# Kernel tuning notes

Hardware: AMD Instinct MI355X
Metric: run time of the kernel (lower is better)

Reference implementation:

```python
import jax, jax.numpy as jnp
import numpy as np

B, S, C, HEADS, EXP = 8, 1024, 256, 8, 4
H = W = 32  # S = H*W
HID = EXP * C
RATES = (1, 6, 12, 18)
EPS = 1e-5


def _conv(x, w, b=None, dilation=1, padding=0):
    out = jax.lax.conv_general_dilated(
        x, w, (1, 1), [(padding, padding), (padding, padding)],
        rhs_dilation=(dilation, dilation),
        dimension_numbers=('NCHW', 'OIHW', 'NCHW'))
    if b is not None:
        out = out + b[None, :, None, None]
    return out


def _bn(x, g, b, m, v):
    # inference-mode BatchNorm2d
    s = (g / jnp.sqrt(v + EPS))[None, :, None, None]
    return (x - m[None, :, None, None]) * s + b[None, :, None, None]


def _ln(x, g, b):
    mu = jnp.mean(x, -1, keepdims=True)
    var = jnp.mean((x - mu) ** 2, -1, keepdims=True)
    return (x - mu) / jnp.sqrt(var + EPS) * g + b


def setup_inputs() -> dict:
    key = jax.random.key(0)
    ks = iter(jax.random.split(key, 64))

    def n(shape, s=0.05):
        return jax.random.normal(next(ks), shape, jnp.float32) * s

    def u(shape):
        return jax.random.uniform(next(ks), shape, jnp.float32, 0.5, 1.5)

    inp = {
        'value': n((B, S, C), 1.0),
        'key': n((B, S, C), 1.0),
        'query': n((B, S, C), 1.0),
        'res': n((B, S, C), 1.0),
        # nn.MultiheadAttention params
        'attn_wi': n((3 * C, C)), 'attn_bi': jnp.zeros((3 * C,)),
        'attn_wo': n((C, C)), 'attn_bo': jnp.zeros((C,)),
        # Modulator params
        'mod_bias': jnp.zeros((1, C, 1, 1)),
        'ca_w1': n((C // 16, C)), 'ca_w2': n((C, C // 16)),
        'pa_w': n((C, C, 1, 1)),
        'pa_bn_g': jnp.ones((C,)), 'pa_bn_b': jnp.zeros((C,)),
        'pa_bn_m': n((C,), 0.1), 'pa_bn_v': u((C,)),
        'sa_w': n((4, C, C, 3, 3)), 'sa_b': jnp.zeros((4, C)),
        'sa_bn_g': jnp.ones((4, C)), 'sa_bn_b': jnp.zeros((4, C)),
        'sa_bn_m': n((4, C), 0.1), 'sa_bn_v': u((4, C)),
        'sa_out_w': n((C, 4 * C, 1, 1)), 'sa_out_b': jnp.zeros((C,)),
        'out_w': n((C, C, 1, 1)), 'out_b': jnp.zeros((C,)),
        'out_bn_g': jnp.ones((C,)), 'out_bn_b': jnp.zeros((C,)),
        'out_bn_m': n((C,), 0.1), 'out_bn_v': u((C,)),
        # LayerNorms
        'ln1_g': jnp.ones((C,)), 'ln1_b': jnp.zeros((C,)),
        'ln2_g': jnp.ones((C,)), 'ln2_b': jnp.zeros((C,)),
        # E_MLP params
        'mlp_w1': n((HID, C)), 'mlp_b1': jnp.zeros((HID,)),
        'dw_w': n((HID, HID, 3, 3), 0.02), 'dw_b': jnp.zeros((HID,)),
        'pw_w': n((HID, HID, 3, 3), 0.02), 'pw_b': jnp.zeros((HID,)),
        'mlp_w2': n((C, HID)), 'mlp_b2': jnp.zeros((C,)),
    }
    return inp


def reference(value, key, query, res,
              attn_wi, attn_bi, attn_wo, attn_bo,
              mod_bias, ca_w1, ca_w2, pa_w,
              pa_bn_g, pa_bn_b, pa_bn_m, pa_bn_v,
              sa_w, sa_b, sa_bn_g, sa_bn_b, sa_bn_m, sa_bn_v,
              sa_out_w, sa_out_b, out_w, out_b,
              out_bn_g, out_bn_b, out_bn_m, out_bn_v,
              ln1_g, ln1_b, ln2_g, ln2_b,
              mlp_w1, mlp_b1, dw_w, dw_b, pw_w, pw_b, mlp_w2, mlp_b2):
    d = C // HEADS
    # SMA arg shuffle: block calls sma(query,key,value) -> SMA(value=query,key=key,query=value)
    # -> nn.MultiheadAttention(query=value_blk, key=key_blk, value=query_blk)
    q = (value @ attn_wi[:C].T + attn_bi[:C]).reshape(B, S, HEADS, d)
    k = (key @ attn_wi[C:2 * C].T + attn_bi[C:2 * C]).reshape(B, S, HEADS, d)
    v = (query @ attn_wi[2 * C:].T + attn_bi[2 * C:]).reshape(B, S, HEADS, d)
    scores = jnp.einsum('bqhd,bkhd->bhqk', q, k) / jnp.sqrt(jnp.float32(d))
    attn = jax.nn.softmax(scores, axis=-1)
    ctx = jnp.einsum('bhqk,bkhd->bqhd', attn, v).reshape(B, S, C)
    msa = ctx @ attn_wo.T + attn_bo                       # [B,S,C]

    x = msa.transpose(0, 2, 1).reshape(B, C, H, W)        # [B,C,H,W]

    # --- Modulator ---
    pa = x * jax.nn.sigmoid(_bn(_conv(x, pa_w), pa_bn_g, pa_bn_b, pa_bn_m, pa_bn_v))
    y = jnp.mean(x, axis=(2, 3))                          # [B,C]
    y = jax.nn.sigmoid(jax.nn.relu(y @ ca_w1.T) @ ca_w2.T)
    ca = x * y[:, :, None, None]
    pa_ca = jax.nn.softmax(pa @ ca, axis=-1)              # [B,C,H,H] (H==W)
    sa_outs = [_bn(jax.nn.relu(_conv(x, sa_w[i], sa_b[i], dilation=r, padding=r)),
                   sa_bn_g[i], sa_bn_b[i], sa_bn_m[i], sa_bn_v[i])
               for i, r in enumerate(RATES)]
    sa = _conv(jnp.concatenate(sa_outs, axis=1), sa_out_w, sa_out_b)
    out = pa_ca @ sa                                      # [B,C,H,W]
    out = _bn(_conv(out, out_w, out_b), out_bn_g, out_bn_b, out_bn_m, out_bn_v)
    syn = out + mod_bias + x                              # residual inside modulator

    attn_seq = syn.reshape(B, C, S).transpose(0, 2, 1)    # [B,S,C]
    q2 = _ln(attn_seq + res, ln1_g, ln1_b)

    # --- E_MLP ---
    h = jax.nn.gelu(q2 @ mlp_w1.T + mlp_b1, approximate=False)  # [B,S,4C]
    hc = h.transpose(0, 2, 1).reshape(B, HID, H, W)
    hc = _conv(hc, dw_w, dw_b, padding=1)
    hc = _conv(hc, pw_w, pw_b, padding=1)
    h2 = hc.reshape(B, HID, S).transpose(0, 2, 1)
    ff = h2 @ mlp_w2.T + mlp_b2
    return _ln(ff + q2, ln2_g, ln2_b)
```

## Files before the change

kernel.cpp:

```cpp
#include <hip/hip_runtime.h>
#include <hip/hip_bf16.h>
#include <math.h>

typedef __attribute__((ext_vector_type(8))) short bf16x8;
typedef __attribute__((ext_vector_type(4))) short bf16x4;
typedef __attribute__((ext_vector_type(4))) float f32x4;

#define MM 8192
#define CC 256

__device__ __forceinline__ short f2bf(float f) {
  unsigned u = __float_as_uint(f);
  u = (u + 0x7FFFu + ((u >> 16) & 1u)) >> 16;
  return (short)u;
}

__device__ __forceinline__ void gload16(const short* g, short* l) {
  __builtin_amdgcn_global_load_lds(
      (const __attribute__((address_space(1))) unsigned int*)(g),
      (__attribute__((address_space(3))) unsigned int*)(l), 16, 0, 0);
}

__global__ __launch_bounds__(256, 2) void convh_k(const short* __restrict__ Ain,
                                                  const short* __restrict__ Wt,
                                                  short* __restrict__ outB,
                                                  const float* __restrict__ bias) {
  extern __shared__ short sm[];
  const int tid = threadIdx.x;
  const int bx = blockIdx.x;
  const int bm = bx & 63, bn = bx >> 6;
  const int l = tid & 63, w = tid >> 6;
  const int wm = w >> 1, wn = w & 1;
  const int lr = l & 15, lg = l >> 4;
  const int lsub = l >> 3;
  const int srcu = (l & 7) ^ lsub;
  const int img = bm >> 3, rbase = (bm & 7) * 4;
  const bf16x8 zv = {0, 0, 0, 0, 0, 0, 0, 0};

  f32x4 acc[4][4];
#pragma unroll
  for (int i = 0; i < 4; ++i)
#pragma unroll
    for (int j = 0; j < 4; ++j) acc[i][j] = (f32x4){0.f, 0.f, 0.f, 0.f};

  const short* wsrc[4];
#pragma unroll
  for (int i = 0; i < 4; ++i) {
    int rowi = (w * 4 + i) * 8 + lsub;
    wsrc[i] = Wt + (size_t)(bn * 128 + rowi) * 1024 + srcu * 8;
  }

  const short* asrc[6]; int apos[6]; bool avalid[6];
#pragma unroll
  for (int i = 0; i < 6; ++i) {
    int ug = tid + i * 256;
    int pos = ug >> 3, u = ug & 7;
    int irow = pos >> 5, px = pos & 31;
    int grow = rbase + irow - 1;
    avalid[i] = ((unsigned)grow < 32u);
    int growc = grow < 0 ? 0 : (grow > 31 ? 31 : grow);
    asrc[i] = Ain + ((size_t)(img * 1024 + growc * 32 + px)) * 1024 + u * 8;
    apos[i] = pos * 64 + ((u ^ (pos & 7)) << 3);
  }

  bf16x8 areg[6];
  auto issueA = [&](int kc) {
#pragma unroll
    for (int i = 0; i < 6; ++i)
      areg[i] = *(const bf16x8*)(asrc[i] + kc * 64);
  };
  auto writeA = [&](int ab) {
    short* abuf = sm + 16384 + ab * 12288;
#pragma unroll
    for (int i = 0; i < 6; ++i)
      *(bf16x8*)(abuf + apos[i]) = avalid[i] ? areg[i] : zv;
  };
  auto issueW = [&](int kc, int tap, int wb) {
    short* base = sm + wb * 8192;
    size_t wo = (size_t)tap * 1048576 + (size_t)kc * 64;
#pragma unroll
    for (int i = 0; i < 4; ++i)
      gload16(wsrc[i] + wo, base + (w * 4 + i) * 512);
  };
  auto compute = [&](int dy, int dx, const short* bA, const short* bB) {
    __builtin_amdgcn_s_setprio(1);
#pragma unroll
    for (int ks = 0; ks < 64; ks += 32) {
      const int u = (ks >> 3) + lg;
      bf16x8 af[4], bfr[4];
#pragma unroll
      for (int mt = 0; mt < 4; ++mt) {
        int px = (mt & 1) * 16 + lr;
        int ipx = px + dx;
        bool okx = ((unsigned)ipx < 32u);
        int pos = (wm * 2 + (mt >> 1) + 1 + dy) * 32 + (ipx & 31);
        bf16x8 v = *(const bf16x8*)&bA[pos * 64 + ((u ^ (pos & 7)) << 3)];
        af[mt] = okx ? v : zv;
      }
#pragma unroll
      for (int nt = 0; nt < 4; ++nt)
        bfr[nt] = *(const bf16x8*)&bB[(wn * 64 + nt * 16 + lr) * 64 + ((u ^ (lr & 7)) << 3)];
#pragma unroll
      for (int mt = 0; mt < 4; ++mt)
#pragma unroll
        for (int nt = 0; nt < 4; ++nt)
          acc[mt][nt] = __builtin_amdgcn_mfma_f32_16x16x32_bf16(af[mt], bfr[nt], acc[mt][nt], 0, 0, 0);
    }
    __builtin_amdgcn_s_setprio(0);
  };

  issueA(0);
  issueW(0, 0, 0);
  issueW(0, 1, 1);
  asm volatile("s_waitcnt vmcnt(4)" ::: "memory");
  writeA(0);
  asm volatile("s_waitcnt lgkmcnt(0)" ::: "memory");

  for (int kc = 0; kc < 16; ++kc) {
    const int ab = kc & 1;
    const short* bA = sm + 16384 + ab * 12288;
#pragma unroll
    for (int tap = 0; tap < 9; ++tap) {
      const int wb = (kc + tap) & 1;
      const short* bB = sm + wb * 8192;
      if (tap == 7) {
        if (kc < 15) asm volatile("s_waitcnt vmcnt(10)" ::: "memory");
        else         asm volatile("s_waitcnt vmcnt(4)" ::: "memory");
      } else if (tap == 8) {
        if (kc < 15) asm volatile("s_waitcnt vmcnt(4)" ::: "memory");
        else         asm volatile("s_waitcnt vmcnt(0)" ::: "memory");
      } else {
        asm volatile("s_waitcnt vmcnt(4)" ::: "memory");
      }
      asm volatile("s_barrier" ::: "memory");
      compute(tap / 3 - 1, tap % 3 - 1, bA, bB);
      asm volatile("s_barrier" ::: "memory");
      if (tap <= 6) {
        if (tap == 6 && kc < 15) issueA(kc + 1);
        issueW(kc, tap + 2, wb);
      } else if (tap == 7) {
        if (kc < 15) issueW(kc + 1, 0, wb);
      } else {
        if (kc < 15) {
          writeA(ab ^ 1);
          asm volatile("s_waitcnt lgkmcnt(0)" ::: "memory");
          issueW(kc + 1, 1, wb);
        }
      }
    }
  }

#pragma unroll
  for (int nt = 0; nt < 4; ++nt) {
    const int col = bn * 128 + wn * 64 + nt * 16 + lr;
    const float bi = bias[col];
#pragma unroll
    for (int mt = 0; mt < 4; ++mt) {
      const int row0 = bm * 128 + wm * 64 + mt * 16 + lg * 4;
#pragma unroll
      for (int j = 0; j < 4; ++j)
        outB[(size_t)(row0 + j) * 1024 + col] = f2bf(acc[mt][nt][j] + bi);
    }
  }
}

struct GP {
  const short* A; const short* W; float* outF; short* outB;
  const float* bias; const float* scale; const float* shift; const float* aux;
  const short* zero;
  long aZStride, wZStride, oZStride;
  int N, Kc, ldA, ldOut, outColOff, outZOff;
  int dil0, dil1, dil2, dil3;
  int T, nkcs;
};

template<int TAPS, int EPI, int OUTMODE>
__global__ __launch_bounds__(256, 2) void gemmd_k(GP p) {
  extern __shared__ short sm[];
  const int tid = threadIdx.x;
  const int bx = blockIdx.x, bz = blockIdx.z;
  const int bm = bx & 63, bn = bx >> 6;
  const int l = tid & 63, w = tid >> 6;
  const int wm = w >> 1, wn = w & 1;
  const int lr = l & 15, lg = l >> 4;
  const int lsub = l >> 3;
  const int srcu = (l & 7) ^ lsub;

  const short* Abase = p.A + (size_t)bz * p.aZStride;
  const short* Wbase = p.W + (size_t)bz * p.wZStride;
  const int dil = (TAPS == 9)
      ? (bz == 0 ? p.dil0 : bz == 1 ? p.dil1 : bz == 2 ? p.dil2 : p.dil3) : 1;

  f32x4 acc[4][4];
#pragma unroll
  for (int i = 0; i < 4; ++i)
#pragma unroll
    for (int j = 0; j < 4; ++j) acc[i][j] = (f32x4){0.f, 0.f, 0.f, 0.f};

  int rowi[4], prow[4], bimg[4], py[4], px[4];
  const short* wsrc[4];
#pragma unroll
  for (int i = 0; i < 4; ++i) {
    rowi[i] = (w * 4 + i) * 8 + lsub;
    prow[i] = bm * 128 + rowi[i];
    bimg[i] = prow[i] >> 10; py[i] = (prow[i] >> 5) & 31; px[i] = prow[i] & 31;
    wsrc[i] = Wbase + (size_t)(bn * 128 + rowi[i]) * p.Kc + srcu * 8;
  }
  const size_t wTap = (size_t)p.N * p.Kc;
  const int nkcMask = (1 << p.nkcs) - 1;

  auto issue = [&](int t, int buf) {
    const int tap = t >> p.nkcs;
    const int kc = t & nkcMask;
    short* base = sm + buf * 16384;
    if (TAPS == 1) {
#pragma unroll
      for (int i = 0; i < 4; ++i)
        gload16(Abase + (size_t)prow[i] * p.ldA + kc * 64 + srcu * 8,
                base + (w * 4 + i) * 512);
    } else {
      const int dy = (tap / 3 - 1) * dil, dx = (tap % 3 - 1) * dil;
#pragma unroll
      for (int i = 0; i < 4; ++i) {
        int yy = py[i] + dy, xx = px[i] + dx;
        bool ok = ((unsigned)yy < 32u) & ((unsigned)xx < 32u);
        const short* a = ok
            ? Abase + (size_t)((bimg[i] << 10) + (yy << 5) + xx) * p.ldA + kc * 64
            : p.zero;
        gload16(a + srcu * 8, base + (w * 4 + i) * 512);
      }
    }
    short* bbase = base + 8192;
    const size_t wo = (size_t)tap * wTap + kc * 64;
#pragma unroll
    for (int i = 0; i < 4; ++i)
      gload16(wsrc[i] + wo, bbase + (w * 4 + i) * 512);
  };

  auto compute = [&](int buf) {
    const short* bA = sm + buf * 16384;
    const short* bB = bA + 8192;
    __builtin_amdgcn_s_setprio(1);
#pragma unroll
    for (int ks = 0; ks < 64; ks += 32) {
      const int u = (ks >> 3) + lg;
      bf16x8 af[4], bfr[4];
#pragma unroll
      for (int mt = 0; mt < 4; ++mt)
        af[mt] = *(bf16x8*)&bA[(wm * 64 + mt * 16 + lr) * 64 + ((u ^ (lr & 7)) << 3)];
#pragma unroll
      for (int nt = 0; nt < 4; ++nt)
        bfr[nt] = *(bf16x8*)&bB[(wn * 64 + nt * 16 + lr) * 64 + ((u ^ (lr & 7)) << 3)];
#pragma unroll
      for (int mt = 0; mt < 4; ++mt)
#pragma unroll
        for (int nt = 0; nt < 4; ++nt)
          acc[mt][nt] = __builtin_amdgcn_mfma_f32_16x16x32_bf16(af[mt], bfr[nt], acc[mt][nt], 0, 0, 0);
    }
    __builtin_amdgcn_s_setprio(0);
  };

  issue(0, 0);
  if (p.T > 1) issue(1, 1);
  int cur = 0;
  for (int t = 0; t < p.T; ++t) {
    if (t + 1 < p.T) asm volatile("s_waitcnt vmcnt(8)" ::: "memory");
    else             asm volatile("s_waitcnt vmcnt(0)" ::: "memory");
    asm volatile("s_barrier" ::: "memory");
    compute(cur);
    asm volatile("s_barrier" ::: "memory");
    if (t + 2 < p.T) issue(t + 2, cur);
    cur ^= 1;
  }

  float* outF = p.outF + (size_t)bz * p.oZStride;
  short* outB = p.outB + (size_t)bz * p.oZStride;
#pragma unroll
  for (int nt = 0; nt < 4; ++nt) {
    const int col = bn * 128 + wn * 64 + nt * 16 + lr;
    const int gcol = p.outColOff + bz * p.outZOff + col;
    const float bi = (p.bias != nullptr) ? p.bias[bz * p.N + col] : 0.f;
    float scl = 0.f, shf = 0.f;
    if (EPI == 3 || EPI == 4 || EPI == 5) {
      scl = p.scale[bz * p.N + col]; shf = p.shift[bz * p.N + col];
    }
#pragma unroll
    for (int mt = 0; mt < 4; ++mt) {
      const int row0 = bm * 128 + wm * 64 + mt * 16 + lg * 4;
#pragma unroll
      for (int j = 0; j < 4; ++j) {
        const long row = row0 + j;
        float v = acc[mt][nt][j];
        if (EPI == 1 || EPI == 2 || EPI == 3) v += bi;
        if (EPI == 2) v = 0.5f * v * (1.f + erff(v * 0.70710678118654752f));
        if (EPI == 3) { v = fmaxf(v, 0.f); v = v * scl + shf; }
        if (EPI == 4) {
          float t2 = v * scl + shf;
          float sg = 1.f / (1.f + __expf(-t2));
          v = p.aux[row * 256 + col] * sg;
        }
        if (EPI == 5) v = v * scl + shf + p.aux[row * 256 + col];
        if (OUTMODE == 0 || OUTMODE == 2) outF[row * (long)p.ldOut + gcol] = v;
        if (OUTMODE == 1 || OUTMODE == 2) outB[row * (long)p.ldOut + gcol] = f2bf(v);
      }
    }
  }
}

__global__ __launch_bounds__(256) void attn_k(const short* qb, const short* kb,
                                              const short* vb, short* ctx) {
  __shared__ short lK[128 * 40];
  __shared__ short lVt[32 * 136];
  __shared__ short lP[4][16 * 136];
  const int tid = threadIdx.x;
  const int qt = blockIdx.x;
  const int bh = blockIdx.y;
  const int b = bh >> 3, h = bh & 7;
  const int l = tid & 63, wv = tid >> 6;
  const int lr = l & 15, lg = l >> 4;
  const float SC = 0.17677669529663687f;

  const int qrow = qt * 64 + wv * 16 + lr;
  const bf16x8 qf = *(const bf16x8*)(qb + ((size_t)(b * 1024 + qrow)) * 256 + h * 32 + lg * 8);

  f32x4 o0 = {0.f,0.f,0.f,0.f}, o1 = {0.f,0.f,0.f,0.f};
  float m[4] = {-1e30f, -1e30f, -1e30f, -1e30f};
  float lsum[4] = {0.f, 0.f, 0.f, 0.f};

  for (int ch = 0; ch < 8; ++ch) {
    __syncthreads();
    {
      const int keyi = tid >> 1, d0 = (tid & 1) * 16;
      const short* src = kb + ((size_t)(b * 1024 + ch * 128 + keyi)) * 256 + h * 32 + d0;
      short* dst = &lK[keyi * 40 + d0];
      *(bf16x8*)dst = *(const bf16x8*)src;
      *(bf16x8*)(dst + 8) = *(const bf16x8*)(src + 8);
    }
    {
      const int keyi = tid >> 1, d0 = (tid & 1) * 16;
      const short* src = vb + ((size_t)(b * 1024 + ch * 128 + keyi)) * 256 + h * 32 + d0;
      short tmp[16];
      *(bf16x8*)tmp = *(const bf16x8*)src;
      *(bf16x8*)(tmp + 8) = *(const bf16x8*)(src + 8);
#pragma unroll
      for (int j = 0; j < 16; ++j) lVt[(d0 + j) * 136 + keyi] = tmp[j];
    }
    __syncthreads();

    f32x4 sc[8];
#pragma unroll
    for (int jt = 0; jt < 8; ++jt) {
      bf16x8 bfr = *(bf16x8*)&lK[(jt * 16 + lr) * 40 + lg * 8];
      sc[jt] = __builtin_amdgcn_mfma_f32_16x16x32_bf16(qf, bfr, (f32x4){0.f,0.f,0.f,0.f}, 0, 0, 0);
      sc[jt] *= SC;
    }
#pragma unroll
    for (int j = 0; j < 4; ++j) {
      float rm = -1e30f;
#pragma unroll
      for (int jt = 0; jt < 8; ++jt) rm = fmaxf(rm, sc[jt][j]);
      rm = fmaxf(rm, __shfl_xor(rm, 1));
      rm = fmaxf(rm, __shfl_xor(rm, 2));
      rm = fmaxf(rm, __shfl_xor(rm, 4));
      rm = fmaxf(rm, __shfl_xor(rm, 8));
      float mn = fmaxf(m[j], rm);
      float alpha = exp2f((m[j] - mn) * 1.44269504088896f);
      m[j] = mn;
      float rs = 0.f;
#pragma unroll
      for (int jt = 0; jt < 8; ++jt) {
        float pv = exp2f((sc[jt][j] - mn) * 1.44269504088896f);
        sc[jt][j] = pv;
        rs += pv;
      }
      rs += __shfl_xor(rs, 1); rs += __shfl_xor(rs, 2);
      rs += __shfl_xor(rs, 4); rs += __shfl_xor(rs, 8);
      lsum[j] = lsum[j] * alpha + rs;
      o0[j] *= alpha; o1[j] *= alpha;
      const int prw = lg * 4 + j;
#pragma unroll
      for (int jt = 0; jt < 8; ++jt) lP[wv][prw * 136 + jt * 16 + lr] = f2bf(sc[jt][j]);
    }
#pragma unroll
    for (int kc = 0; kc < 4; ++kc) {
      bf16x8 pf = *(bf16x8*)&lP[wv][lr * 136 + kc * 32 + lg * 8];
      bf16x8 v0 = *(bf16x8*)&lVt[lr * 136 + kc * 32 + lg * 8];
      bf16x8 v1 = *(bf16x8*)&lVt[(16 + lr) * 136 + kc * 32 + lg * 8];
      o0 = __builtin_amdgcn_mfma_f32_16x16x32_bf16(pf, v0, o0, 0, 0, 0);
      o1 = __builtin_amdgcn_mfma_f32_16x16x32_bf16(pf, v1, o1, 0, 0, 0);
    }
  }
  const size_t orow = (size_t)(b * 1024 + qt * 64 + wv * 16);
#pragma unroll
  for (int j = 0; j < 4; ++j) {
    float inv = 1.f / lsum[j];
    ctx[(orow + lg * 4 + j) * 256 + h * 32 + lr]      = f2bf(o0[j] * inv);
    ctx[(orow + lg * 4 + j) * 256 + h * 32 + 16 + lr] = f2bf(o1[j] * inv);
  }
}

__global__ __launch_bounds__(256) void cvt4_k(const float* src, short* dst, int n4) {
  int i = blockIdx.x * 256 + threadIdx.x;
  if (i < n4) {
    f32x4 v = ((const f32x4*)src)[i];
    bf16x4 o;
    o[0] = f2bf(v[0]); o[1] = f2bf(v[1]); o[2] = f2bf(v[2]); o[3] = f2bf(v[3]);
    ((bf16x4*)dst)[i] = o;
  }
}

__global__ __launch_bounds__(256) void zero_k(short* p) {
  p[blockIdx.x * 256 + threadIdx.x] = 0;
}

__global__ __launch_bounds__(256) void tap_k(const float* src, short* dst, int n) {
  int i = blockIdx.x * 256 + threadIdx.x;
  if (i >= n) return;
  const float* s = src + (size_t)i * 9;
  float v[9];
#pragma unroll
  for (int t = 0; t < 9; ++t) v[t] = s[t];
#pragma unroll
  for (int t = 0; t < 9; ++t) dst[(size_t)t * n + i] = f2bf(v[t]);
}

__global__ void bnprep_k(const float* pg, const float* pb, const float* pm, const float* pv,
                         const float* sg, const float* sb, const float* sm, const float* sv,
                         const float* og, const float* ob, const float* om, const float* ov,
                         const float* conv_ob, const float* mbias, float* out) {
  int c = threadIdx.x;
  float s = pg[c] / sqrtf(pv[c] + 1e-5f);
  out[c] = s;
  out[256 + c] = pb[c] - pm[c] * s;
  for (int i = 0; i < 4; ++i) {
    int idx = i * 256 + c;
    float ss = sg[idx] / sqrtf(sv[idx] + 1e-5f);
    out[512 + idx] = ss;
    out[1536 + idx] = sb[idx] - sm[idx] * ss;
  }
  float os = og[c] / sqrtf(ov[c] + 1e-5f);
  out[2560 + c] = os;
  out[2816 + c] = ob[c] - om[c] * os + conv_ob[c] * os + mbias[c];
}

__global__ __launch_bounds__(256) void tposef_k(const float* src, float* dst) {
  __shared__ float tile[32][33];
  int pc = blockIdx.x, cc = blockIdx.y, b = blockIdx.z;
  int tx = threadIdx.x & 31, ty = threadIdx.x >> 5;
  const float* s = src + ((size_t)b * 1024 + pc * 32) * 256 + cc * 32;
#pragma unroll
  for (int k = 0; k < 4; ++k)
    tile[ty + 8 * k][tx] = s[(ty + 8 * k) * 256 + tx];
  __syncthreads();
  float* d = dst + ((size_t)b * 256 + cc * 32) * 1024 + pc * 32;
#pragma unroll
  for (int k = 0; k < 4; ++k)
    d[(ty + 8 * k) * 1024 + tx] = tile[tx][ty + 8 * k];
}

__global__ __launch_bounds__(256) void tposeb_k(const float* src, short* dst) {
  __shared__ float tile[32][33];
  int pc = blockIdx.x, cc = blockIdx.y, b = blockIdx.z;
  int tx = threadIdx.x & 31, ty = threadIdx.x >> 5;
  const float* s = src + ((size_t)b * 256 + cc * 32) * 1024 + pc * 32;
#pragma unroll
  for (int k = 0; k < 4; ++k)
    tile[ty + 8 * k][tx] = s[(ty + 8 * k) * 1024 + tx];
  __syncthreads();
  short* d = dst + ((size_t)b * 1024 + pc * 32) * 256 + cc * 32;
#pragma unroll
  for (int k = 0; k < 4; ++k)
    d[(ty + 8 * k) * 256 + tx] = f2bf(tile[tx][ty + 8 * k]);
}

__global__ __launch_bounds__(256) void camean_k(const float* x, float* partial) {
  int blk = blockIdx.x, c = threadIdx.x;
  const float* px = x + ((size_t)blk * 64) * 256 + c;
  float s = 0.f;
#pragma unroll 4
  for (int r = 0; r < 64; ++r) s += px[(size_t)r * 256];
  partial[blk * 256 + c] = s;
}

__global__ __launch_bounds__(256) void ca2_k(const float* partial, const float* w1,
                                             const float* w2, float* y2) {
  __shared__ float ly[256];
  __shared__ float ly1[16];
  int b = blockIdx.x, c = threadIdx.x;
  float s = 0.f;
#pragma unroll
  for (int j = 0; j < 16; ++j) s += partial[(b * 16 + j) * 256 + c];
  ly[c] = s * (1.f / 1024.f);
  __syncthreads();
  if (c < 16) {
    float a = 0.f;
    const float* wp = w1 + c * 256;
    for (int i = 0; i < 256; ++i) a += ly[i] * wp[i];
    ly1[c] = fmaxf(a, 0.f);
  }
  __syncthreads();
  float a = 0.f;
  const float* wp = w2 + c * 16;
#pragma unroll
  for (int j = 0; j < 16; ++j) a += ly1[j] * wp[j];
  y2[b * 256 + c] = 1.f / (1.f + __expf(-a));
}

__global__ __launch_bounds__(256) void bm1_k(const float* paT, const float* xT,
                                             const float* y2, float* pa_ca) {
  __shared__ float sp[32][33], sx[32][33], so[32][33];
  __shared__ float rinv[32];
  int bc = blockIdx.x, t = threadIdx.x;
  for (int e = t; e < 1024; e += 256) {
    sp[e >> 5][e & 31] = paT[(size_t)bc * 1024 + e];
    sx[e >> 5][e & 31] = xT[(size_t)bc * 1024 + e];
  }
  __syncthreads();
  float yv = y2[bc];
  int i = t >> 3, j0 = (t & 7) * 4;
  float a0 = 0.f, a1 = 0.f, a2 = 0.f, a3 = 0.f;
  for (int k = 0; k < 32; ++k) {
    float pv = sp[i][k];
    a0 += pv * sx[k][j0];     a1 += pv * sx[k][j0 + 1];
    a2 += pv * sx[k][j0 + 2]; a3 += pv * sx[k][j0 + 3];
  }
  so[i][j0] = a0 * yv; so[i][j0 + 1] = a1 * yv;
  so[i][j0 + 2] = a2 * yv; so[i][j0 + 3] = a3 * yv;
  __syncthreads();
  if (t < 32) {
    float mx = -1e30f;
    for (int j = 0; j < 32; ++j) mx = fmaxf(mx, so[t][j]);
    float sum = 0.f;
    for (int j = 0; j < 32; ++j) { float pp = __expf(so[t][j] - mx); so[t][j] = pp; sum += pp; }
    rinv[t] = 1.f / sum;
  }
  __syncthreads();
  for (int e = t; e < 1024; e += 256)
    pa_ca[(size_t)bc * 1024 + e] = so[e >> 5][e & 31] * rinv[e >> 5];
}

__global__ __launch_bounds__(256) void bm2_k(const float* pa_ca, const float* saT, float* moT) {
  __shared__ float sp[32][33], ss[32][33];
  int bc = blockIdx.x, t = threadIdx.x;
  for (int e = t; e < 1024; e += 256) {
    sp[e >> 5][e & 31] = pa_ca[(size_t)bc * 1024 + e];
    ss[e >> 5][e & 31] = saT[(size_t)bc * 1024 + e];
  }
  __syncthreads();
  int i = t >> 3, j0 = (t & 7) * 4;
  float a0 = 0.f, a1 = 0.f, a2 = 0.f, a3 = 0.f;
  for (int k = 0; k < 32; ++k) {
    float pv = sp[i][k];
    a0 += pv * ss[k][j0];     a1 += pv * ss[k][j0 + 1];
    a2 += pv * ss[k][j0 + 2]; a3 += pv * ss[k][j0 + 3];
  }
  size_t base = (size_t)bc * 1024 + i * 32 + j0;
  moT[base] = a0; moT[base + 1] = a1; moT[base + 2] = a2; moT[base + 3] = a3;
}

template<int DUAL>
__global__ __launch_bounds__(256) void ln_k(const float* in, const float* res,
                                            const float* g, const float* bta,
                                            float* out, short* outB) {
  __shared__ float red[8];
  size_t row = blockIdx.x;
  int c = threadIdx.x;
  int wv = c >> 6, lane = c & 63;
  float v = in[row * 256 + c] + res[row * 256 + c];
  float s = v;
  for (int mk = 1; mk < 64; mk <<= 1) s += __shfl_xor(s, mk);
  if (lane == 0) red[wv] = s;
  __syncthreads();
  float mu = (red[0] + red[1] + red[2] + red[3]) * (1.f / 256.f);
  float d = v - mu;
  float q = d * d;
  for (int mk = 1; mk < 64; mk <<= 1) q += __shfl_xor(q, mk);
  if (lane == 0) red[4 + wv] = q;
  __syncthreads();
  float var = (red[4] + red[5] + red[6] + red[7]) * (1.f / 256.f);
  float o = d * rsqrtf(var + 1e-5f) * g[c] + bta[c];
  out[row * 256 + c] = o;
  if (DUAL) outB[row * 256 + c] = f2bf(o);
}

extern "C" void kernel_launch(void* const* d_in, const int* in_sizes, int n_in,
                              void* d_out, int out_size, void* d_ws, size_t ws_size,
                              hipStream_t stream) {
  (void)in_sizes; (void)n_in; (void)out_size; (void)ws_size;
  const float* value    = (const float*)d_in[0];
  const float* key      = (const float*)d_in[1];
  const float* query    = (const float*)d_in[2];
  const float* res      = (const float*)d_in[3];
  const float* attn_wi  = (const float*)d_in[4];
  const float* attn_bi  = (const float*)d_in[5];
  const float* attn_wo  = (const float*)d_in[6];
  const float* attn_bo  = (const float*)d_in[7];
  const float* mod_bias = (const float*)d_in[8];
  const float* ca_w1    = (const float*)d_in[9];
  const float* ca_w2    = (const float*)d_in[10];
  const float* pa_w     = (const float*)d_in[11];
  const float* pa_bn_g  = (const float*)d_in[12];
  const float* pa_bn_b  = (const float*)d_in[13];
  const float* pa_bn_m  = (const float*)d_in[14];
  const float* pa_bn_v  = (const float*)d_in[15];
  const float* sa_w     = (const float*)d_in[16];
  const float* sa_b     = (const float*)d_in[17];
  const float* sa_bn_g  = (const float*)d_in[18];
  const float* sa_bn_b  = (const float*)d_in[19];
  const float* sa_bn_m  = (const float*)d_in[20];
  const float* sa_bn_v  = (const float*)d_in[21];
  const float* sa_out_w = (const float*)d_in[22];
  const float* sa_out_b = (const float*)d_in[23];
  const float* out_w    = (const float*)d_in[24];
  const float* out_b    = (const float*)d_in[25];
  const float* out_bn_g = (const float*)d_in[26];
  const float* out_bn_b = (const float*)d_in[27];
  const float* out_bn_m = (const float*)d_in[28];
  const float* out_bn_v = (const float*)d_in[29];
  const float* ln1_g    = (const float*)d_in[30];
  const float* ln1_b    = (const float*)d_in[31];
  const float* ln2_g    = (const float*)d_in[32];
  const float* ln2_b    = (const float*)d_in[33];
  const float* mlp_w1   = (const float*)d_in[34];
  const float* mlp_b1   = (const float*)d_in[35];
  const float* dw_w     = (const float*)d_in[36];
  const float* dw_b     = (const float*)d_in[37];
  const float* pw_w     = (const float*)d_in[38];
  const float* pw_b     = (const float*)d_in[39];
  const float* mlp_w2   = (const float*)d_in[40];
  const float* mlp_b2   = (const float*)d_in[41];

  char* ws = (char*)d_ws;
  const size_t MB = 1024 * 1024;
  char* A = ws + 0 * MB;
  char* Bx = ws + 16 * MB;
  char* Cx = ws + 32 * MB;
  float* xbuf  = (float*)(ws + 40 * MB);
  short* xbf   = (short*)(ws + 48 * MB);
  char* Fx = ws + 52 * MB;
  float* q2buf = (float*)(ws + 60 * MB);
  short* q2B   = (short*)(ws + 68 * MB);
  short* wdw   = (short*)(ws + 72 * MB);
  short* wpw   = (short*)(ws + 90 * MB);
  size_t o = 108 * MB;
  short* w_awi  = (short*)(ws + o); o += 768 * 256 * 2;
  short* w_awo  = (short*)(ws + o); o += 256 * 256 * 2;
  short* w_pa   = (short*)(ws + o); o += 256 * 256 * 2;
  short* w_sa   = (short*)(ws + o); o += (size_t)4 * 9 * 256 * 256 * 2;
  short* w_saou = (short*)(ws + o); o += 256 * 1024 * 2;
  short* w_out  = (short*)(ws + o); o += 256 * 256 * 2;
  short* w_mlp1 = (short*)(ws + o); o += 1024 * 256 * 2;
  short* w_mlp2 = (short*)(ws + o); o += 256 * 1024 * 2;
  float* bn     = (float*)(ws + o); o += 3072 * 4;
  float* y2buf  = (float*)(ws + o); o += 8 * 256 * 4;
  float* capart = (float*)(ws + o); o += 128 * 256 * 4;
  short* zbuf   = (short*)(ws + o); o += 2048 * 2;

  short* vkq  = (short*)A;
  short* qkv  = (short*)Bx;
  short* ctxB = (short*)Cx;
  float* xT   = (float*)A;
  float* paT  = (float*)(A + 8 * MB);
  float* paBuf = (float*)Cx;
  float* pa_ca = (float*)Bx;
  float* saBuf = (float*)(Bx + 8 * MB);
  short* saCat = (short*)A;
  float* saT  = (float*)Cx;
  float* moT  = (float*)Fx;
  short* modB = (short*)Cx;
  float* synBuf = (float*)Fx;
  short* hB   = (short*)A;
  short* hc1B = (short*)Bx;
  short* h2B  = (short*)A;
  float* ffBuf = (float*)Cx;

  const int LDSB = 2 * 16384 * 2;
  const int LDSC = 40960 * 2;
  hipFuncSetAttribute((const void*)gemmd_k<1, 1, 1>, hipFuncAttributeMaxDynamicSharedMemorySize, LDSB);
  hipFuncSetAttribute((const void*)gemmd_k<1, 1, 2>, hipFuncAttributeMaxDynamicSharedMemorySize, LDSB);
  hipFuncSetAttribute((const void*)gemmd_k<1, 4, 0>, hipFuncAttributeMaxDynamicSharedMemorySize, LDSB);
  hipFuncSetAttribute((const void*)gemmd_k<9, 3, 1>, hipFuncAttributeMaxDynamicSharedMemorySize, LDSB);
  hipFuncSetAttribute((const void*)gemmd_k<1, 1, 0>, hipFuncAttributeMaxDynamicSharedMemorySize, LDSB);
  hipFuncSetAttribute((const void*)gemmd_k<1, 5, 0>, hipFuncAttributeMaxDynamicSharedMemorySize, LDSB);
  hipFuncSetAttribute((const void*)gemmd_k<1, 2, 1>, hipFuncAttributeMaxDynamicSharedMemorySize, LDSB);
  hipFuncSetAttribute((const void*)convh_k, hipFuncAttributeMaxDynamicSharedMemorySize, LDSC);

  zero_k<<<8, 256, 0, stream>>>(zbuf);
  cvt4_k<<<192, 256, 0, stream>>>(attn_wi, w_awi, 768 * 64);
  cvt4_k<<<64, 256, 0, stream>>>(attn_wo, w_awo, 256 * 64);
  cvt4_k<<<64, 256, 0, stream>>>(pa_w, w_pa, 256 * 64);
  for (int i4 = 0; i4 < 4; ++i4)
    tap_k<<<256, 256, 0, stream>>>(sa_w + (size_t)i4 * 589824,
                                   w_sa + (size_t)i4 * 589824, 65536);
  cvt4_k<<<256, 256, 0, stream>>>(sa_out_w, w_saou, 1024 * 64);
  cvt4_k<<<64, 256, 0, stream>>>(out_w, w_out, 256 * 64);
  cvt4_k<<<256, 256, 0, stream>>>(mlp_w1, w_mlp1, 1024 * 64);
  cvt4_k<<<256, 256, 0, stream>>>(mlp_w2, w_mlp2, 1024 * 64);
  tap_k<<<4096, 256, 0, stream>>>(dw_w, wdw, 1048576);
  tap_k<<<4096, 256, 0, stream>>>(pw_w, wpw, 1048576);
  bnprep_k<<<1, 256, 0, stream>>>(pa_bn_g, pa_bn_b, pa_bn_m, pa_bn_v,
                                  sa_bn_g, sa_bn_b, sa_bn_m, sa_bn_v,
                                  out_bn_g, out_bn_b, out_bn_m, out_bn_v,
                                  out_b, mod_bias, bn);
  cvt4_k<<<2048, 256, 0, stream>>>(value, vkq, MM * 64);
  cvt4_k<<<2048, 256, 0, stream>>>(key,   vkq + (size_t)MM * 256, MM * 64);
  cvt4_k<<<2048, 256, 0, stream>>>(query, vkq + (size_t)2 * MM * 256, MM * 64);

  GP g;
  g.zero = zbuf; g.scale = nullptr; g.shift = nullptr; g.aux = nullptr;
  g.aZStride = 0; g.wZStride = 0; g.oZStride = 0;
  g.outColOff = 0; g.outZOff = 0;
  g.dil0 = 1; g.dil1 = 1; g.dil2 = 1; g.dil3 = 1;
  g.outF = nullptr; g.outB = nullptr;

  g.A = vkq; g.W = w_awi; g.outB = qkv; g.bias = attn_bi;
  g.N = 256; g.Kc = 256; g.ldA = 256; g.ldOut = 256; g.T = 4; g.nkcs = 2;
  g.aZStride = (size_t)MM * 256; g.wZStride = 256 * 256; g.oZStride = (size_t)MM * 256;
  gemmd_k<1, 1, 1><<<dim3(128, 1, 3), 256, LDSB, stream>>>(g);
  g.aZStride = 0; g.wZStride = 0; g.oZStride = 0;

  attn_k<<<dim3(16, 64), 256, 0, stream>>>(qkv, qkv + (size_t)MM * 256,
                                           qkv + (size_t)2 * MM * 256, ctxB);

  g.A = ctxB; g.W = w_awo; g.outF = xbuf; g.outB = xbf; g.bias = attn_bo;
  gemmd_k<1, 1, 2><<<dim3(128), 256, LDSB, stream>>>(g);

  tposef_k<<<dim3(32, 8, 8), 256, 0, stream>>>(xbuf, xT);

  g.A = xbf; g.W = w_pa; g.outF = paBuf; g.outB = nullptr; g.bias = nullptr;
  g.scale = bn; g.shift = bn + 256; g.aux = xbuf;
  gemmd_k<1, 4, 0><<<dim3(128), 256, LDSB, stream>>>(g);
  g.scale = nullptr; g.shift = nullptr; g.aux = nullptr;
  tposef_k<<<dim3(32, 8, 8), 256, 0, stream>>>(paBuf, paT);

  camean_k<<<128, 256, 0, stream>>>(xbuf, capart);
  ca2_k<<<8, 256, 0, stream>>>(capart, ca_w1, ca_w2, y2buf);
  bm1_k<<<2048, 256, 0, stream>>>(paT, xT, y2buf, pa_ca);

  g.A = xbf; g.W = w_sa; g.outB = saCat; g.outF = nullptr;
  g.bias = sa_b; g.scale = bn + 512; g.shift = bn + 1536;
  g.ldOut = 1024; g.outZOff = 256; g.wZStride = (size_t)9 * 256 * 256;
  g.dil0 = 1; g.dil1 = 6; g.dil2 = 12; g.dil3 = 18;
  g.T = 36; g.nkcs = 2;
  gemmd_k<9, 3, 1><<<dim3(128, 1, 4), 256, LDSB, stream>>>(g);
  g.outZOff = 0; g.wZStride = 0; g.scale = nullptr; g.shift = nullptr;
  g.dil0 = 1; g.dil1 = 1; g.dil2 = 1; g.dil3 = 1;

  g.A = saCat; g.W = w_saou; g.outF = saBuf; g.outB = nullptr; g.bias = sa_out_b;
  g.N = 256; g.Kc = 1024; g.ldA = 1024; g.ldOut = 256; g.T = 16; g.nkcs = 4;
  gemmd_k<1, 1, 0><<<dim3(128), 256, LDSB, stream>>>(g);
  tposef_k<<<dim3(32, 8, 8), 256, 0, stream>>>(saBuf, saT);

  bm2_k<<<2048, 256, 0, stream>>>(pa_ca, saT, moT);
  tposeb_k<<<dim3(32, 8, 8), 256, 0, stream>>>(moT, modB);

  g.A = modB; g.W = w_out; g.outF = synBuf; g.bias = nullptr;
  g.scale = bn + 2560; g.shift = bn + 2816; g.aux = xbuf;
  g.N = 256; g.Kc = 256; g.ldA = 256; g.ldOut = 256; g.T = 4; g.nkcs = 2;
  gemmd_k<1, 5, 0><<<dim3(128), 256, LDSB, stream>>>(g);
  g.scale = nullptr; g.shift = nullptr; g.aux = nullptr;

  ln_k<1><<<8192, 256, 0, stream>>>(synBuf, res, ln1_g, ln1_b, q2buf, q2B);

  g.A = q2B; g.W = w_mlp1; g.outB = hB; g.outF = nullptr; g.bias = mlp_b1;
  g.N = 1024; g.Kc = 256; g.ldA = 256; g.ldOut = 1024; g.T = 4; g.nkcs = 2;
  gemmd_k<1, 2, 1><<<dim3(512), 256, LDSB, stream>>>(g);

  convh_k<<<dim3(512), 256, LDSC, stream>>>(hB, wdw, hc1B, dw_b);

  convh_k<<<dim3(512), 256, LDSC, stream>>>(hc1B, wpw, h2B, pw_b);

  g.A = h2B; g.W = w_mlp2; g.outF = ffBuf; g.outB = nullptr; g.bias = mlp_b2;
  g.N = 256; g.Kc = 1024; g.ldA = 1024; g.ldOut = 256; g.T = 16; g.nkcs = 4;
  gemmd_k<1, 1, 0><<<dim3(128), 256, LDSB, stream>>>(g);

  ln_k<0><<<8192, 256, 0, stream>>>(ffBuf, q2buf, ln2_g, ln2_b, (float*)d_out, nullptr);
}
```

Measured before the change: 579.4 us.

## Load conv weights directly into registers, drop LDS weight staging and barriers

In the 3x3 conv kernel, the weight B-fragments are now read from global memory straight into registers, double-buffered across taps, instead of being staged through LDS with async global-to-LDS loads. Only the activation tile stays in static LDS, which cuts LDS use and removes the two barriers per tap, leaving one barrier per K chunk. Each lane now issues its own uncoalesced-ish 16-byte global loads and needs 16 extra vector registers. It also relies on the compiler's waitcnt placement instead of explicit vmcnt tuning, which may expose global load latency and limit occupancy.

```diff
diff --git a/kernel.cpp b/kernel.cpp
--- a/kernel.cpp
+++ b/kernel.cpp
@@ -25,15 +25,13 @@
                                                   const short* __restrict__ Wt,
                                                   short* __restrict__ outB,
                                                   const float* __restrict__ bias) {
-  extern __shared__ short sm[];
+  __shared__ short sA[2][12288];
   const int tid = threadIdx.x;
   const int bx = blockIdx.x;
   const int bm = bx & 63, bn = bx >> 6;
   const int l = tid & 63, w = tid >> 6;
   const int wm = w >> 1, wn = w & 1;
   const int lr = l & 15, lg = l >> 4;
-  const int lsub = l >> 3;
-  const int srcu = (l & 7) ^ lsub;
   const int img = bm >> 3, rbase = (bm & 7) * 4;
   const bf16x8 zv = {0, 0, 0, 0, 0, 0, 0, 0};
 
@@ -43,12 +41,7 @@
 #pragma unroll
     for (int j = 0; j < 4; ++j) acc[i][j] = (f32x4){0.f, 0.f, 0.f, 0.f};
 
-  const short* wsrc[4];
-#pragma unroll
-  for (int i = 0; i < 4; ++i) {
-    int rowi = (w * 4 + i) * 8 + lsub;
-    wsrc[i] = Wt + (size_t)(bn * 128 + rowi) * 1024 + srcu * 8;
-  }
+  const short* wlane = Wt + (size_t)(bn * 128 + wn * 64 + lr) * 1024 + lg * 8;
 
   const short* asrc[6]; int apos[6]; bool avalid[6];
 #pragma unroll
@@ -70,84 +63,74 @@
       areg[i] = *(const bf16x8*)(asrc[i] + kc * 64);
   };
   auto writeA = [&](int ab) {
-    short* abuf = sm + 16384 + ab * 12288;
+    short* abuf = &sA[ab][0];
 #pragma unroll
     for (int i = 0; i < 6; ++i)
       *(bf16x8*)(abuf + apos[i]) = avalid[i] ? areg[i] : zv;
   };
-  auto issueW = [&](int kc, int tap, int wb) {
-    short* base = sm + wb * 8192;
-    size_t wo = (size_t)tap * 1048576 + (size_t)kc * 64;
-#pragma unroll
-    for (int i = 0; i < 4; ++i)
-      gload16(wsrc[i] + wo, base + (w * 4 + i) * 512);
+
+  auto loadW = [&](bf16x8* dst, int tap, int kc) {
+    const short* wp = wlane + (size_t)tap * 1048576 + (size_t)kc * 64;
+#pragma unroll
+    for (int nt = 0; nt < 4; ++nt)
+#pragma unroll
+      for (int kh = 0; kh < 2; ++kh)
+        dst[nt * 2 + kh] = *(const bf16x8*)(wp + nt * 16384 + kh * 32);
   };
-  auto compute = [&](int dy, int dx, const short* bA, const short* bB) {
+
+  auto computeT = [&](int dy, int dx, const short* bA, const bf16x8* wf) {
     __builtin_amdgcn_s_setprio(1);
 #pragma unroll
-    for (int ks = 0; ks < 64; ks += 32) {
-      const int u = (ks >> 3) + lg;
-      bf16x8 af[4], bfr[4];
+    for (int kh = 0; kh < 2; ++kh) {
+      const int u0 = kh * 4 + lg;
+      bf16x8 af[4];
 #pragma unroll
       for (int mt = 0; mt < 4; ++mt) {
         int px = (mt & 1) * 16 + lr;
         int ipx = px + dx;
         bool okx = ((unsigned)ipx < 32u);
         int pos = (wm * 2 + (mt >> 1) + 1 + dy) * 32 + (ipx & 31);
-        bf16x8 v = *(const bf16x8*)&bA[pos * 64 + ((u ^ (pos & 7)) << 3)];
+        bf16x8 v = *(const bf16x8*)&bA[pos * 64 + ((u0 ^ (pos & 7)) << 3)];
         af[mt] = okx ? v : zv;
       }
 #pragma unroll
-      for (int nt = 0; nt < 4; ++nt)
-        bfr[nt] = *(const bf16x8*)&bB[(wn * 64 + nt * 16 + lr) * 64 + ((u ^ (lr & 7)) << 3)];
-#pragma unroll
       for (int mt = 0; mt < 4; ++mt)
 #pragma unroll
         for (int nt = 0; nt < 4; ++nt)
-          acc[mt][nt] = __builtin_amdgcn_mfma_f32_16x16x32_bf16(af[mt], bfr[nt], acc[mt][nt], 0, 0, 0);
+          acc[mt][nt] = __builtin_amdgcn_mfma_f32_16x16x32_bf16(af[mt], wf[nt * 2 + kh], acc[mt][nt], 0, 0, 0);
     }
     __builtin_amdgcn_s_setprio(0);
   };
 
+  bf16x8 wrA[8], wrB[8];
+
+  auto kcBody = [&](int kc, const short* bA, int abw, bf16x8* wEv, bf16x8* wOd) {
+    const int kcn = kc < 15 ? kc + 1 : 15;
+#pragma unroll
+    for (int tap = 0; tap < 9; ++tap) {
+      bf16x8* cur = (tap & 1) ? wOd : wEv;
+      computeT(tap / 3 - 1, tap % 3 - 1, bA, cur);
+      if (tap == 0) issueA(kcn);
+      if (tap <= 6)      loadW(cur, tap + 2, kc);
+      else if (tap == 7) loadW(cur, 0, kcn);
+      else               loadW(cur, 1, kcn);
+      if (tap == 5) writeA(abw);
+    }
+    asm volatile("s_waitcnt lgkmcnt(0)" ::: "memory");
+    __builtin_amdgcn_s_barrier();
+  };
+
   issueA(0);
-  issueW(0, 0, 0);
-  issueW(0, 1, 1);
-  asm volatile("s_waitcnt vmcnt(4)" ::: "memory");
+  loadW(wrA, 0, 0);
+  loadW(wrB, 1, 0);
   writeA(0);
   asm volatile("s_waitcnt lgkmcnt(0)" ::: "memory");
-
-  for (int kc = 0; kc < 16; ++kc) {
-    const int ab = kc & 1;
-    const short* bA = sm + 16384 + ab * 12288;
-#pragma unroll
-    for (int tap = 0; tap < 9; ++tap) {
-      const int wb = (kc + tap) & 1;
-      const short* bB = sm + wb * 8192;
-      if (tap == 7) {
-        if (kc < 15) asm volatile("s_waitcnt vmcnt(10)" ::: "memory");
-        else         asm volatile("s_waitcnt vmcnt(4)" ::: "memory");
-      } else if (tap == 8) {
-        if (kc < 15) asm volatile("s_waitcnt vmcnt(4)" ::: "memory");
-        else         asm volatile("s_waitcnt vmcnt(0)" ::: "memory");
-      } else {
-        asm volatile("s_waitcnt vmcnt(4)" ::: "memory");
-      }
-      asm volatile("s_barrier" ::: "memory");
-      compute(tap / 3 - 1, tap % 3 - 1, bA, bB);
-      asm volatile("s_barrier" ::: "memory");
-      if (tap <= 6) {
-        if (tap == 6 && kc < 15) issueA(kc + 1);
-        issueW(kc, tap + 2, wb);
-      } else if (tap == 7) {
-        if (kc < 15) issueW(kc + 1, 0, wb);
-      } else {
-        if (kc < 15) {
-          writeA(ab ^ 1);
-          asm volatile("s_waitcnt lgkmcnt(0)" ::: "memory");
-          issueW(kc + 1, 1, wb);
-        }
-      }
-    }
+  __builtin_amdgcn_s_barrier();
+
+#pragma unroll 1
+  for (int k2 = 0; k2 < 8; ++k2) {
+    kcBody(2 * k2,     &sA[0][0], 1, wrA, wrB);
+    kcBody(2 * k2 + 1, &sA[1][0], 0, wrB, wrA);
   }
 
 #pragma unroll
@@ -675,7 +658,6 @@
   float* ffBuf = (float*)Cx;
 
   const int LDSB = 2 * 16384 * 2;
-  const int LDSC = 40960 * 2;
   hipFuncSetAttribute((const void*)gemmd_k<1, 1, 1>, hipFuncAttributeMaxDynamicSharedMemorySize, LDSB);
   hipFuncSetAttribute((const void*)gemmd_k<1, 1, 2>, hipFuncAttributeMaxDynamicSharedMemorySize, LDSB);
   hipFuncSetAttribute((const void*)gemmd_k<1, 4, 0>, hipFuncAttributeMaxDynamicSharedMemorySize, LDSB);
@@ -683,7 +665,6 @@
   hipFuncSetAttribute((const void*)gemmd_k<1, 1, 0>, hipFuncAttributeMaxDynamicSharedMemorySize, LDSB);
   hipFuncSetAttribute((const void*)gemmd_k<1, 5, 0>, hipFuncAttributeMaxDynamicSharedMemorySize, LDSB);
   hipFuncSetAttribute((const void*)gemmd_k<1, 2, 1>, hipFuncAttributeMaxDynamicSharedMemorySize, LDSB);
-  hipFuncSetAttribute((const void*)convh_k, hipFuncAttributeMaxDynamicSharedMemorySize, LDSC);
 
   zero_k<<<8, 256, 0, stream>>>(zbuf);
   cvt4_k<<<192, 256, 0, stream>>>(attn_wi, w_awi, 768 * 64);
@@ -766,9 +747,9 @@
   g.N = 1024; g.Kc = 256; g.ldA = 256; g.ldOut = 1024; g.T = 4; g.nkcs = 2;
   gemmd_k<1, 2, 1><<<dim3(512), 256, LDSB, stream>>>(g);
 
-  convh_k<<<dim3(512), 256, LDSC, stream>>>(hB, wdw, hc1B, dw_b);
-
-  convh_k<<<dim3(512), 256, LDSC, stream>>>(hc1B, wpw, h2B, pw_b);
+  convh_k<<<dim3(512), 256, 0, stream>>>(hB, wdw, hc1B, dw_b);
+
+  convh_k<<<dim3(512), 256, 0, stream>>>(hc1B, wpw, h2B, pw_b);
 
   g.A = h2B; g.W = w_mlp2; g.outF = ffBuf; g.outB = nullptr; g.bias = mlp_b2;
   g.N = 256; g.Kc = 1024; g.ldA = 1024; g.ldOut = 256; g.T = 16; g.nkcs = 4;
```

Result: slower. 872.6 us (+50.6%).
